# Kernel tuning notes

Hardware: AMD Instinct MI355X
Metric: run time of the kernel (lower is better)

## Reference

```python
import jax, jax.numpy as jnp
import numpy as np

TEMPERATURE = 0.5


def setup_inputs() -> dict:
    key = jax.random.key(0)
    ks = jax.random.split(key, 12)
    B, N, T = 128, 64, 256
    IN, H, OUT = N + T, 256, 128
    E = N * (N - 1) // 2  # 2016 upper-tri edges per graph
    total_edges = B * E
    inp = {
        "x_topology": jax.random.normal(ks[0], (B, N, N), jnp.float32),
        "x_temporal": jax.random.normal(ks[1], (B, N, T), jnp.float32),
        "gumbel_u": jax.random.uniform(ks[2], (total_edges,), jnp.float32, 1e-6, 1.0),
        # GNNLayer linear
        "W_gnn": jax.random.normal(ks[3], (IN, H), jnp.float32) / np.sqrt(IN),
        "b_gnn": jnp.zeros((H,), jnp.float32),
        # edge heads (input dim 2*H)
        "W_mean": jax.random.normal(ks[4], (2 * H, OUT), jnp.float32) / np.sqrt(2 * H),
        "b_mean": jnp.zeros((OUT,), jnp.float32),
        "W_var": jax.random.normal(ks[5], (2 * H, OUT), jnp.float32) / np.sqrt(2 * H),
        "b_var": jnp.zeros((OUT,), jnp.float32),
        "W_w": jax.random.normal(ks[6], (2 * H, 1), jnp.float32) / np.sqrt(2 * H),
        "b_w": jnp.zeros((1,), jnp.float32),
    }
    return inp


def reference(x_topology, x_temporal, gumbel_u, W_gnn, b_gnn,
              W_mean, b_mean, W_var, b_var, W_w, b_w):
    B, N, _ = x_topology.shape
    T = x_temporal.shape[-1]
    # Upper-triangular fully-connected edge index (no self loops), batched with node offsets.
    row, col = jnp.triu_indices(N, k=1)          # [E]
    E = row.shape[0]
    offs = (jnp.arange(B) * N)[:, None]          # [B,1]
    src = (row[None, :] + offs).reshape(-1)       # [B*E]
    dst = (col[None, :] + offs).reshape(-1)       # [B*E]

    # Node features: concat topology + temporal, flatten batch of graphs.
    x = jnp.concatenate([x_topology, x_temporal], axis=-1).reshape(B * N, N + T)

    # Mean aggregation (PyG aggr='mean'): messages x[src] scattered to dst; 0 for isolated nodes.
    msg_sum = jax.ops.segment_sum(x[src], dst, num_segments=B * N)      # [B*N, N+T]
    cnt = jax.ops.segment_sum(jnp.ones_like(src, x.dtype), dst, num_segments=B * N)
    agg = jnp.where(cnt[:, None] > 0, msg_sum / jnp.maximum(cnt, 1.0)[:, None], 0.0)

    h = jax.nn.relu(agg @ W_gnn + b_gnn)          # [B*N, H]

    # Edge MLP heads on gathered [src||dst] embeddings.
    ef = jnp.concatenate([h[src], h[dst]], axis=-1)        # [B*E, 2H]
    mean = ef @ W_mean + b_mean                             # [B*E, OUT]
    variance = jax.nn.softplus(ef @ W_var + b_var) + 1e-6   # [B*E, OUT]
    weight = jax.nn.sigmoid((ef @ W_w + b_w)[:, 0])          # [B*E]

    # Gumbel-softmax over the flattened edge-weight vector (dim=-1 of a 1-D tensor).
    g = -jnp.log(-jnp.log(gumbel_u))
    gumbel_w = jax.nn.softmax((weight + g) / TEMPERATURE, axis=-1)

    # Gaussian similarity per edge, scatter into dense adjacency.
    sim = jnp.exp(-0.5 * jnp.mean(mean ** 2 / (variance + 1e-8), axis=-1))
    edge_w = sim * gumbel_w                                  # [B*E]

    b_idx = jnp.repeat(jnp.arange(B), E)
    adj = jnp.zeros((B, N, N), x.dtype).at[b_idx, jnp.tile(row, B), jnp.tile(col, B)].set(edge_w)
    return adj
```

## Files before the change

kernel.cpp:

```cpp
#include <hip/hip_runtime.h>
#include <hip/hip_bf16.h>
#include <math.h>

#define Bg   128
#define Nn   64
#define Tt   256
#define INF  320
#define Hd   256
#define OUTD 128
#define Ee   2016
#define TOTE (Bg*Ee)
#define SCOLS 576
#define MROWS 8192

typedef __attribute__((ext_vector_type(8))) short bf16x8;
typedef __attribute__((ext_vector_type(4))) float f32x4;

static __device__ __forceinline__ ushort f2bf(float v) {
    __hip_bfloat16 h = __float2bfloat16(v);
    return *(ushort*)&h;
}

#define CVT_N (INF * Hd)
#define PACK_N (Hd * SCOLS)
__global__ void k_prep(const float* __restrict__ Wg, const float* __restrict__ Wm,
                       const float* __restrict__ Wv, const float* __restrict__ Ww,
                       const float* __restrict__ bm, const float* __restrict__ bv,
                       const float* __restrict__ bw,
                       ushort* __restrict__ WgbT, ushort* __restrict__ WcatT,
                       float* __restrict__ ebias, unsigned* __restrict__ red) {
    int idx = blockIdx.x * 256 + threadIdx.x;
    if (idx == 0) { red[0] = 0u; red[1] = 0u; }
    if (idx < CVT_N) {
        int n = idx / INF, k = idx - n * INF;
        WgbT[idx] = f2bf(Wg[k * Hd + n]);
        return;
    }
    idx -= CVT_N;
    if (idx < PACK_N) {
        int n = idx / Hd, k = idx - n * Hd;
        float v = 0.f;
        if (n < 128)       v = Wm[k * 128 + n];
        else if (n < 256)  v = Wm[(256 + k) * 128 + (n - 128)];
        else if (n < 384)  v = Wv[k * 128 + (n - 256)];
        else if (n < 512)  v = Wv[(256 + k) * 128 + (n - 384)];
        else if (n == 512) v = Ww[k];
        else if (n == 513) v = Ww[256 + k];
        WcatT[idx] = f2bf(v);
        return;
    }
    idx -= PACK_N;
    if (idx >= SCOLS) return;
    float e = 0.f;
    if (idx < 128)                    e = bm[idx];
    else if (idx >= 256 && idx < 384) e = bv[idx - 256];
    else if (idx == 512)              e = bw[0];
    ebias[idx] = e;
}

__global__ __launch_bounds__(256) void k_agg(const float* __restrict__ topo,
                                             const float* __restrict__ temp,
                                             ushort* __restrict__ agg) {
    __shared__ float T[64 * 65];
    const int b = blockIdx.x, ft = blockIdx.y;
    const int tid = threadIdx.x;
    const int row = tid >> 2, seg = tid & 3;
    const float* src = (ft == 0) ? (topo + (size_t)(b * Nn + row) * Nn)
                                 : (temp + (size_t)(b * Nn + row) * Tt + (ft - 1) * 64);
    #pragma unroll
    for (int i = 0; i < 4; ++i) {
        float4 v = *(const float4*)(src + seg * 16 + i * 4);
        float* d = &T[row * 65 + seg * 16 + i * 4];
        d[0] = v.x; d[1] = v.y; d[2] = v.z; d[3] = v.w;
    }
    __syncthreads();
    const int w = tid >> 6, lane = tid & 63;
    #pragma unroll
    for (int k = 0; k < 16; ++k) {
        int f = w * 16 + k;
        float x = T[lane * 65 + f];
        float incl = x;
        #pragma unroll
        for (int o = 1; o < 64; o <<= 1) {
            float t = __shfl_up(incl, o);
            if (lane >= o) incl += t;
        }
        float excl = incl - x;
        T[lane * 65 + f] = lane ? excl * __builtin_amdgcn_rcpf((float)lane) : 0.f;
    }
    __syncthreads();
    const int node = tid >> 2, f0 = (tid & 3) * 16;
    ushort tmp[16];
    #pragma unroll
    for (int i = 0; i < 16; ++i) tmp[i] = f2bf(T[node * 65 + f0 + i]);
    ushort* dst = agg + (size_t)(b * Nn + node) * INF + ft * 64 + f0;
    *(uint4*)dst = *(uint4*)tmp;
    *(uint4*)(dst + 8) = *(uint4*)(tmp + 8);
}

__global__ __launch_bounds__(256) void k_gemm_mfma(const ushort* __restrict__ A,
                                                   const ushort* __restrict__ BT,
                                                   const float* __restrict__ bias,
                                                   ushort* __restrict__ Cb,
                                                   float* __restrict__ Cf,
                                                   int N, int K, int relu, int transC) {
    __shared__ ushort Asl[64 * 72];
    __shared__ ushort Bsl[64 * 72];
    const int tid = threadIdx.x;
    const int w = tid >> 6, lane = tid & 63;
    const int quad = lane >> 4, r16 = lane & 15;
    const int m0 = blockIdx.y * 64, n0 = blockIdx.x * 64;
    const int row = tid >> 2, seg = tid & 3;
    f32x4 acc[4] = {};

    for (int k0 = 0; k0 < K; k0 += 64) {
        const ushort* ap = A + (size_t)(m0 + row) * K + k0 + seg * 16;
        uint4 a0 = ((const uint4*)ap)[0];
        uint4 a1 = ((const uint4*)ap)[1];
        *(uint4*)(Asl + row * 72 + seg * 16)     = a0;
        *(uint4*)(Asl + row * 72 + seg * 16 + 8) = a1;
        const ushort* bp = BT + (size_t)(n0 + row) * K + k0 + seg * 16;
        uint4 b0 = ((const uint4*)bp)[0];
        uint4 b1 = ((const uint4*)bp)[1];
        *(uint4*)(Bsl + row * 72 + seg * 16)     = b0;
        *(uint4*)(Bsl + row * 72 + seg * 16 + 8) = b1;
        __syncthreads();

        bf16x8 af0 = *(const bf16x8*)(Asl + (w * 16 + r16) * 72 + quad * 8);
        bf16x8 af1 = *(const bf16x8*)(Asl + (w * 16 + r16) * 72 + 32 + quad * 8);
        #pragma unroll
        for (int ns = 0; ns < 4; ++ns) {
            bf16x8 bf0 = *(const bf16x8*)(Bsl + (ns * 16 + r16) * 72 + quad * 8);
            bf16x8 bf1 = *(const bf16x8*)(Bsl + (ns * 16 + r16) * 72 + 32 + quad * 8);
            acc[ns] = __builtin_amdgcn_mfma_f32_16x16x32_bf16(af0, bf0, acc[ns], 0, 0, 0);
            acc[ns] = __builtin_amdgcn_mfma_f32_16x16x32_bf16(af1, bf1, acc[ns], 0, 0, 0);
        }
        __syncthreads();
    }

    const int row0 = m0 + w * 16 + quad * 4;
    #pragma unroll
    for (int ns = 0; ns < 4; ++ns) {
        f32x4 a = acc[ns];
        int col = n0 + ns * 16 + r16;
        float bb = bias ? bias[col] : 0.f;
        float vv[4];
        #pragma unroll
        for (int i = 0; i < 4; ++i) {
            float v = a[i] + bb;
            if (relu) v = fmaxf(v, 0.f);
            vv[i] = v;
        }
        if (transC) {
            *(float4*)(Cf + (size_t)col * MROWS + row0) = make_float4(vv[0], vv[1], vv[2], vv[3]);
        } else {
            #pragma unroll
            for (int i = 0; i < 4; ++i) {
                int row2 = row0 + i;
                if (Cb) Cb[(size_t)row2 * N + col] = f2bf(vv[i]);
                else    Cf[(size_t)row2 * N + col] = vv[i];
            }
        }
    }
}

static __device__ __forceinline__ float eterm(float pm, float qm, float pv, float qv) {
    float m = pm + qm;
    float x = pv + qv;
    float sp = fmaxf(x, 0.f) + __logf(1.f + __expf(-fabsf(x)));
    return m * m * __builtin_amdgcn_rcpf(sp + 1.01e-6f);
}

__global__ __launch_bounds__(256) void k_edge4(const float* __restrict__ ST,
                                               const float* __restrict__ gu,
                                               float* __restrict__ numer,
                                               unsigned* __restrict__ red) {
    __shared__ float L[4][16][132];
    __shared__ float sm[256];
    const int p = blockIdx.x % 10, b = blockIdx.x / 10;
    const int G0v[10] = {0,0,0,0,1,1,1,2,2,3};
    const int G1v[10] = {0,1,2,3,1,2,3,2,3,3};
    const int g0 = G0v[p], g1 = G1v[p];
    const int tid = threadIdx.x;

    #pragma unroll
    for (int rep = 0; rep < 8; ++rep) {
        int it = tid + 256 * rep;
        int arr = it >> 9;
        int c = (it >> 2) & 127, nq = it & 3;
        int g = (arr & 1) ? g1 : g0;
        float4 v = *(const float4*)&ST[(size_t)(arr * 128 + c) * MROWS + b * 64 + g * 16 + nq * 4];
        L[arr][nq * 4 + 0][c] = v.x;
        L[arr][nq * 4 + 1][c] = v.y;
        L[arr][nq * 4 + 2][c] = v.z;
        L[arr][nq * 4 + 3][c] = v.w;
    }
    __syncthreads();

    const int i = tid >> 4, j = tid & 15;
    float acc = 0.f;
    #pragma unroll 4
    for (int t = 0; t < 128; t += 4) {
        float4 mi = *(const float4*)&L[0][i][t];
        float4 mj = *(const float4*)&L[1][j][t];
        float4 vi = *(const float4*)&L[2][i][t];
        float4 vj = *(const float4*)&L[3][j][t];
        acc += eterm(mi.x, mj.x, vi.x, vj.x);
        acc += eterm(mi.y, mj.y, vi.y, vj.y);
        acc += eterm(mi.z, mj.z, vi.z, vj.z);
        acc += eterm(mi.w, mj.w, vi.w, vj.w);
    }

    const int ni = g0 * 16 + i, nj = g1 * 16 + j;
    float en = 0.f;
    if (ni < nj) {
        int e = b * Ee + (ni * (127 - ni)) / 2 + (nj - ni - 1);
        float se = __expf(acc * (-1.f / 256.f));
        float wr = ST[(size_t)512 * MROWS + b * 64 + ni]
                 + ST[(size_t)513 * MROWS + b * 64 + nj];
        float w  = __builtin_amdgcn_rcpf(1.f + __expf(-wr));
        float g  = -__logf(-__logf(gu[e]));
        en = __expf((w + g) * 2.0f);
        numer[e] = se * en;
    }
    sm[tid] = en; __syncthreads();
    for (int s = 128; s; s >>= 1) {
        if (tid < s) sm[tid] += sm[tid + s];
        __syncthreads();
    }
    if (!tid) atomicAdd((float*)&red[1], sm[0]);
}

__global__ void k_out(const float* __restrict__ numer, const unsigned* __restrict__ red,
                      float* __restrict__ out) {
    int idx = blockIdx.x * 256 + threadIdx.x;
    if (idx >= Bg * Nn * Nn) return;
    int b = idx >> 12;
    int rem = idx & 4095;
    int r = rem >> 6, c = rem & 63;
    float v = 0.f;
    if (c > r) {
        int e = b * Ee + (r * (127 - r)) / 2 + (c - r - 1);
        float Sinv = __builtin_amdgcn_rcpf(((const float*)red)[1]);
        v = numer[e] * Sinv;
    }
    out[idx] = v;
}

extern "C" void kernel_launch(void* const* d_in, const int* in_sizes, int n_in,
                              void* d_out, int out_size, void* d_ws, size_t ws_size,
                              hipStream_t stream) {
    const float* topo = (const float*)d_in[0];
    const float* temp = (const float*)d_in[1];
    const float* gu   = (const float*)d_in[2];
    const float* Wg   = (const float*)d_in[3];
    const float* bg   = (const float*)d_in[4];
    const float* Wm   = (const float*)d_in[5];
    const float* bm   = (const float*)d_in[6];
    const float* Wv   = (const float*)d_in[7];
    const float* bv   = (const float*)d_in[8];
    const float* Ww   = (const float*)d_in[9];
    const float* bw   = (const float*)d_in[10];
    float* out = (float*)d_out;

    char* ws = (char*)d_ws;
    size_t off = 0;
    auto carve = [&](size_t bytes) { char* p = ws + off; off = (off + bytes + 255) & ~(size_t)255; return p; };

    char*   r1    = carve((size_t)SCOLS * MROWS * 4);
    float*  ST    = (float*)r1;
    ushort* aggb  = (ushort*)r1;
    ushort* hb    = (ushort*)carve((size_t)MROWS * Hd * 2);
    ushort* WgbT  = (ushort*)carve((size_t)INF * Hd * 2);
    ushort* WcatT = (ushort*)carve((size_t)Hd * SCOLS * 2);
    float*  ebias = (float*)carve((size_t)SCOLS * 4);
    float*  numer = (float*)carve((size_t)TOTE * 4);
    unsigned* red = (unsigned*)carve(256);

    k_prep<<<(CVT_N + PACK_N + SCOLS + 255) / 256, 256, 0, stream>>>(
        Wg, Wm, Wv, Ww, bm, bv, bw, WgbT, WcatT, ebias, red);
    k_agg<<<dim3(Bg, INF / 64), 256, 0, stream>>>(topo, temp, aggb);
    k_gemm_mfma<<<dim3(Hd / 64, MROWS / 64), 256, 0, stream>>>(
        aggb, WgbT, bg, hb, nullptr, Hd, INF, 1, 0);
    k_gemm_mfma<<<dim3(SCOLS / 64, MROWS / 64), 256, 0, stream>>>(
        hb, WcatT, ebias, nullptr, ST, SCOLS, Hd, 0, 1);
    k_edge4<<<Bg * 10, 256, 0, stream>>>(ST, gu, numer, red);
    k_out<<<(Bg * Nn * Nn + 255) / 256, 256, 0, stream>>>(numer, red, out);
}
```

Before: 149.1 us.

## Fold log2 scaling into GEMM epilogue and compact edge kernel work

The edge-head GEMM epilogue now pre-scales the mean columns by 1/sqrt(ln2) and the variance columns by log2(e). This lets the per-edge softplus use native exp2/log2 intrinsics with an adjusted epsilon instead of expf/logf. The edge kernel also skips the idle lower-triangle pairs in diagonal tiles, loads the feature dimension in two halves so less shared memory is used and occupancy can rise, swizzles block IDs so each XCD gets a contiguous range of graphs, and replaces the shared-memory tree reduction with a wavefront shuffle reduction. The folded scaling changes the arithmetic slightly, and diagonal tiles now leave more than half their threads idle.

```diff
diff --git a/kernel.cpp b/kernel.cpp
--- a/kernel.cpp
+++ b/kernel.cpp
@@ -12,6 +12,10 @@
 #define TOTE (Bg*Ee)
 #define SCOLS 576
 #define MROWS 8192
+
+#define RSQRT_LN2 1.2011224087864498f
+#define LOG2E     1.4426950408889634f
+#define EPS_T     1.45719e-6f
 
 typedef __attribute__((ext_vector_type(8))) short bf16x8;
 typedef __attribute__((ext_vector_type(4))) float f32x4;
@@ -103,7 +107,8 @@
                                                    const float* __restrict__ bias,
                                                    ushort* __restrict__ Cb,
                                                    float* __restrict__ Cf,
-                                                   int N, int K, int relu, int transC) {
+                                                   int N, int K, int relu, int transC,
+                                                   int edgeScale) {
     __shared__ ushort Asl[64 * 72];
     __shared__ ushort Bsl[64 * 72];
     const int tid = threadIdx.x;
@@ -152,6 +157,11 @@
             vv[i] = v;
         }
         if (transC) {
+            if (edgeScale) {
+                float s = (col < 256) ? RSQRT_LN2 : (col < 512 ? LOG2E : 1.f);
+                #pragma unroll
+                for (int i = 0; i < 4; ++i) vv[i] *= s;
+            }
             *(float4*)(Cf + (size_t)col * MROWS + row0) = make_float4(vv[0], vv[1], vv[2], vv[3]);
         } else {
             #pragma unroll
@@ -166,54 +176,74 @@
 
 static __device__ __forceinline__ float eterm(float pm, float qm, float pv, float qv) {
     float m = pm + qm;
-    float x = pv + qv;
-    float sp = fmaxf(x, 0.f) + __logf(1.f + __expf(-fabsf(x)));
-    return m * m * __builtin_amdgcn_rcpf(sp + 1.01e-6f);
-}
-
-__global__ __launch_bounds__(256) void k_edge4(const float* __restrict__ ST,
-                                               const float* __restrict__ gu,
-                                               float* __restrict__ numer,
-                                               unsigned* __restrict__ red) {
-    __shared__ float L[4][16][132];
-    __shared__ float sm[256];
-    const int p = blockIdx.x % 10, b = blockIdx.x / 10;
+    float y = pv + qv;
+    float e = __builtin_amdgcn_exp2f(-__builtin_fabsf(y));
+    float t = fmaxf(y, 0.f) + __builtin_amdgcn_logf(1.f + e)
+            + EPS_T;
+    return m * m * __builtin_amdgcn_rcpf(t);
+}
+
+__global__ __launch_bounds__(256, 8) void k_edge4(const float* __restrict__ ST,
+                                                  const float* __restrict__ gu,
+                                                  float* __restrict__ numer,
+                                                  unsigned* __restrict__ red) {
+    __shared__ float L[4][16][68];
+    __shared__ float sred[4];
+    const int bid = blockIdx.x;
+    const int xcd = bid & 7, k = bid >> 3;
+    const int b = xcd * 16 + k / 10;
+    const int p = k - (k / 10) * 10;
     const int G0v[10] = {0,0,0,0,1,1,1,2,2,3};
     const int G1v[10] = {0,1,2,3,1,2,3,2,3,3};
     const int g0 = G0v[p], g1 = G1v[p];
     const int tid = threadIdx.x;
 
-    #pragma unroll
-    for (int rep = 0; rep < 8; ++rep) {
-        int it = tid + 256 * rep;
-        int arr = it >> 9;
-        int c = (it >> 2) & 127, nq = it & 3;
-        int g = (arr & 1) ? g1 : g0;
-        float4 v = *(const float4*)&ST[(size_t)(arr * 128 + c) * MROWS + b * 64 + g * 16 + nq * 4];
-        L[arr][nq * 4 + 0][c] = v.x;
-        L[arr][nq * 4 + 1][c] = v.y;
-        L[arr][nq * 4 + 2][c] = v.z;
-        L[arr][nq * 4 + 3][c] = v.w;
-    }
-    __syncthreads();
-
-    const int i = tid >> 4, j = tid & 15;
+    int i, j;
+    bool valid;
+    if (g0 != g1) {
+        i = tid >> 4; j = tid & 15; valid = true;
+    } else {
+        valid = tid < 120;
+        int ii = 0, rr = tid;
+        if (valid) { while (rr >= 15 - ii) { rr -= 15 - ii; ++ii; } }
+        i = valid ? ii : 0;
+        j = valid ? (ii + 1 + rr) : 1;
+    }
+
+    const int c = tid >> 2, nq = tid & 3;
     float acc = 0.f;
-    #pragma unroll 4
-    for (int t = 0; t < 128; t += 4) {
-        float4 mi = *(const float4*)&L[0][i][t];
-        float4 mj = *(const float4*)&L[1][j][t];
-        float4 vi = *(const float4*)&L[2][i][t];
-        float4 vj = *(const float4*)&L[3][j][t];
-        acc += eterm(mi.x, mj.x, vi.x, vj.x);
-        acc += eterm(mi.y, mj.y, vi.y, vj.y);
-        acc += eterm(mi.z, mj.z, vi.z, vj.z);
-        acc += eterm(mi.w, mj.w, vi.w, vj.w);
+    #pragma unroll
+    for (int h = 0; h < 2; ++h) {
+        if (h) __syncthreads();
+        #pragma unroll
+        for (int arr = 0; arr < 4; ++arr) {
+            const int g = (arr & 1) ? g1 : g0;
+            float4 v = *(const float4*)&ST[(size_t)((arr << 7) + (h << 6) + c) * MROWS
+                                           + b * 64 + (g << 4) + (nq << 2)];
+            L[arr][nq * 4 + 0][c] = v.x;
+            L[arr][nq * 4 + 1][c] = v.y;
+            L[arr][nq * 4 + 2][c] = v.z;
+            L[arr][nq * 4 + 3][c] = v.w;
+        }
+        __syncthreads();
+        if (valid) {
+            #pragma unroll 4
+            for (int t = 0; t < 64; t += 4) {
+                float4 mi = *(const float4*)&L[0][i][t];
+                float4 mj = *(const float4*)&L[1][j][t];
+                float4 vi = *(const float4*)&L[2][i][t];
+                float4 vj = *(const float4*)&L[3][j][t];
+                acc += eterm(mi.x, mj.x, vi.x, vj.x);
+                acc += eterm(mi.y, mj.y, vi.y, vj.y);
+                acc += eterm(mi.z, mj.z, vi.z, vj.z);
+                acc += eterm(mi.w, mj.w, vi.w, vj.w);
+            }
+        }
     }
 
     const int ni = g0 * 16 + i, nj = g1 * 16 + j;
     float en = 0.f;
-    if (ni < nj) {
+    if (valid) {
         int e = b * Ee + (ni * (127 - ni)) / 2 + (nj - ni - 1);
         float se = __expf(acc * (-1.f / 256.f));
         float wr = ST[(size_t)512 * MROWS + b * 64 + ni]
@@ -223,12 +253,11 @@
         en = __expf((w + g) * 2.0f);
         numer[e] = se * en;
     }
-    sm[tid] = en; __syncthreads();
-    for (int s = 128; s; s >>= 1) {
-        if (tid < s) sm[tid] += sm[tid + s];
-        __syncthreads();
-    }
-    if (!tid) atomicAdd((float*)&red[1], sm[0]);
+    #pragma unroll
+    for (int o = 32; o; o >>= 1) en += __shfl_down(en, o);
+    if ((tid & 63) == 0) sred[tid >> 6] = en;
+    __syncthreads();
+    if (tid == 0) atomicAdd((float*)&red[1], sred[0] + sred[1] + sred[2] + sred[3]);
 }
 
 __global__ void k_out(const float* __restrict__ numer, const unsigned* __restrict__ red,
@@ -281,9 +310,9 @@
         Wg, Wm, Wv, Ww, bm, bv, bw, WgbT, WcatT, ebias, red);
     k_agg<<<dim3(Bg, INF / 64), 256, 0, stream>>>(topo, temp, aggb);
     k_gemm_mfma<<<dim3(Hd / 64, MROWS / 64), 256, 0, stream>>>(
-        aggb, WgbT, bg, hb, nullptr, Hd, INF, 1, 0);
+        aggb, WgbT, bg, hb, nullptr, Hd, INF, 1, 0, 0);
     k_gemm_mfma<<<dim3(SCOLS / 64, MROWS / 64), 256, 0, stream>>>(
-        hb, WcatT, ebias, nullptr, ST, SCOLS, Hd, 0, 1);
+        hb, WcatT, ebias, nullptr, ST, SCOLS, Hd, 0, 1, 1);
     k_edge4<<<Bg * 10, 256, 0, stream>>>(ST, gu, numer, red);
     k_out<<<(Bg * Nn * Nn + 255) / 256, 256, 0, stream>>>(numer, red, out);
 }
```

Result: faster. 135.9 us (-8.9%).
